# Kernel optimization log

Measured on AMD Instinct MI355X. Metric: run time of the kernel, lower is better.

The kernel has to match this reference:

```python
import jax, jax.numpy as jnp
import numpy as np

NEG = -1e10

def setup_inputs() -> dict:
    key = jax.random.key(0)
    ks = jax.random.split(key, 12)
    B, W, V, D, R, VOCAB = 16, 64, 64, 256, 64, 50000
    head_ctx = jax.random.randint(ks[0], (B, W), 0, VOCAB)
    tail_ctx = jax.random.randint(ks[1], (B, V), 0, VOCAB)
    emb = jax.random.normal(ks[2], (VOCAB, D), dtype=jnp.float32) * 0.02
    rela_mat = jax.random.normal(ks[3], (R, D), dtype=jnp.float32) * 0.02
    fc_w = jax.random.normal(ks[4], (3 * D, D), dtype=jnp.float32) * (1.0 / np.sqrt(3 * D))
    fc_b = jnp.zeros((D,), jnp.float32)
    att_w1 = jax.random.normal(ks[5], (D, D), dtype=jnp.float32) * (1.0 / np.sqrt(D))
    att_b1 = jnp.zeros((D,), jnp.float32)
    att_w2 = jax.random.normal(ks[6], (D, 1), dtype=jnp.float32) * (1.0 / np.sqrt(D))
    att_b2 = jnp.zeros((1,), jnp.float32)
    out_w = jax.random.normal(ks[7], (D, 1), dtype=jnp.float32) * (1.0 / np.sqrt(D))
    out_b = jnp.zeros((1,), jnp.float32)
    return {"head_ctx": head_ctx, "tail_ctx": tail_ctx, "emb": emb, "rela_mat": rela_mat,
            "fc_w": fc_w, "fc_b": fc_b, "att_w1": att_w1, "att_b1": att_b1,
            "att_w2": att_w2, "att_b2": att_b2, "out_w": out_w, "out_b": out_b}

def reference(head_ctx, tail_ctx, emb, rela_mat, fc_w, fc_b, att_w1, att_b1, att_w2, att_b2, out_w, out_b):
    A = emb[head_ctx]            # [B, W, D]
    Bt = emb[tail_ctx]           # [B, V, D]
    Bsz, W, D = A.shape
    V = Bt.shape[1]
    R = rela_mat.shape[0]
    N = W * V
    # DistMult scoring for every (head_i, tail_j, rela_r) triple, no repeat materialization
    scores = jnp.einsum('bid,bjd,rd->bijr', A, Bt, rela_mat).reshape(Bsz, N, R)
    # cut_rela_score: mask relations not beating the null (last) relation
    null = scores[:, :, -1:]
    scores = jnp.where(scores <= null, NEG, scores)
    norm_scores = jax.nn.softmax(scores, axis=-1)            # [B, N, R]
    rela_vec = jnp.einsum('bnr,rd->bnd', norm_scores, rela_mat)
    # tuple (i,j) pairing: index n = i*V + j
    A_rep = jnp.broadcast_to(A[:, :, None, :], (Bsz, W, V, D)).reshape(Bsz, N, D)
    B_rep = jnp.broadcast_to(Bt[:, None, :, :], (Bsz, W, V, D)).reshape(Bsz, N, D)
    tuple_vec = jnp.tanh(jnp.concatenate([A_rep, B_rep, rela_vec], axis=-1) @ fc_w + fc_b)  # [B, N, D]
    # tuple attention pooling
    att = jnp.tanh(tuple_vec @ att_w1 + att_b1) @ att_w2 + att_b2   # [B, N, 1]
    att_norms = jax.nn.softmax(att, axis=1)                          # [B, N, 1]
    fuse = jnp.sum(att_norms * tuple_vec, axis=1)                    # [B, D]
    logits = (fuse @ out_w + out_b).squeeze(-1)                      # [B]
    return logits, att_norms, norm_scores
```

## Files before the change

### kernel.cpp

```cpp
#include <hip/hip_runtime.h>
#include <hip/hip_bf16.h>

#define NB 16
#define NW 64
#define NV 64
#define ND 256
#define NR 64
#define NN 4096
#define NEGV -10000000000.0f

typedef __attribute__((ext_vector_type(8))) short short8;
typedef __attribute__((ext_vector_type(4))) float f32x4;

__device__ inline float cvt(const void* p, int idx, int flag) {
  if (flag) return __bfloat162float(((const __hip_bfloat16*)p)[idx]);
  return ((const float*)p)[idx];
}
__device__ inline void stv(void* p, int idx, float v, int flag) {
  if (flag) ((__hip_bfloat16*)p)[idx] = __float2bfloat16(v);
  else ((float*)p)[idx] = v;
}
__device__ inline float bf2f(short s) {
  return __uint_as_float(((unsigned int)(unsigned short)s) << 16);
}
__device__ inline float tanh_fast(float x) {
  float ax = fabsf(x);
  float e = __expf(-2.f * ax);
  float r = (1.f - e) / (1.f + e);
  return copysignf(r, x);
}

__global__ void k_detect(const unsigned int* embw, int* flagp) {
  __shared__ float red[256];
  int t = threadIdx.x;
  float mx = 0.f;
  for (int i = t; i < 1024; i += 256) {
    unsigned int w = embw[i];
    unsigned int fb = (w & 0xffffu) << 16;
    float a = fabsf(__uint_as_float(fb));
    if (!(a < 1e9f)) a = 1e9f;
    mx = fmaxf(mx, a);
  }
  red[t] = mx;
  __syncthreads();
  for (int s = 128; s > 0; s >>= 1) {
    if (t < s) red[t] = fmaxf(red[t], red[t + s]);
    __syncthreads();
  }
  if (t == 0) flagp[0] = (red[0] < 1000.f) ? 1 : 0;
}

__global__ void k_prep(const void* rela, float* relaT,
                       const void* b1, const void* w2, const void* outw,
                       const void* b2, const void* outb, float* sp,
                       const void* w1, __hip_bfloat16* w1b,
                       const int* head, const int* tail, const void* emb,
                       float* Af, float* Bf, const int* flagp) {
  int flag = flagp[0];
  int blk = blockIdx.x;
  int t = threadIdx.x;
  if (blk < 64) {
    relaT[t * NR + blk] = cvt(rela, blk * ND + t, flag);
  } else if (blk == 64) {
    sp[t] = cvt(b1, t, flag);
    sp[256 + t] = cvt(w2, t, flag);
    sp[512 + t] = cvt(outw, t, flag);
    if (t == 0) {
      sp[768] = cvt(b2, 0, flag);
      sp[769] = cvt(outb, 0, flag);
    }
  } else if (blk < 321) {
    int flat = (blk - 65) * 256 + t;
    int i = flat & 7;
    int lane = (flat >> 3) & 63;
    int kst = (flat >> 9) & 7;
    int nt = flat >> 12;
    int k = kst * 32 + (lane >> 4) * 8 + i;
    int n = nt * 16 + (lane & 15);
    w1b[flat] = __float2bfloat16(cvt(w1, k * ND + n, flag));
  } else {
    int row = blk - 321;
    if (row < NB * NW) {
      int ix = head[row];
      Af[row * ND + t] = cvt(emb, ix * ND + t, flag);
    } else {
      int rr = row - NB * NW;
      int ix = tail[rr];
      Bf[rr * ND + t] = cvt(emb, ix * ND + t, flag);
    }
  }
}

__global__ void __launch_bounds__(256) k_premm(const float* __restrict__ Af,
                                               const float* __restrict__ Bf,
                                               const void* __restrict__ rela,
                                               const void* __restrict__ fcw,
                                               const void* __restrict__ fcb,
                                               float* __restrict__ Ah,
                                               float* __restrict__ Bh,
                                               __hip_bfloat16* __restrict__ rwb,
                                               const int* __restrict__ flagp) {
  int flag = flagp[0];
  int blk = blockIdx.x;
  int t = threadIdx.x;
  __shared__ float rl[4][ND];
  int base, wbase, addb = 0, isr = 0;
  const float* src = Af;
  if (blk < 256) { base = blk * 4; wbase = 0; addb = 1; }
  else if (blk < 512) { base = (blk - 256) * 4; src = Bf; wbase = ND; }
  else { base = (blk - 512) * 4; wbase = 2 * ND; isr = 1; }
#pragma unroll
  for (int i = 0; i < 4; ++i)
    rl[i][t] = isr ? cvt(rela, (base + i) * ND + t, flag)
                   : src[(base + i) * ND + t];
  __syncthreads();
  float acc0 = 0.f, acc1 = 0.f, acc2 = 0.f, acc3 = 0.f;
  const f32x4* r0p = (const f32x4*)rl[0];
  const f32x4* r1p = (const f32x4*)rl[1];
  const f32x4* r2p = (const f32x4*)rl[2];
  const f32x4* r3p = (const f32x4*)rl[3];
#pragma unroll 4
  for (int k4 = 0; k4 < 64; ++k4) {
    float w0 = cvt(fcw, (wbase + k4 * 4 + 0) * ND + t, flag);
    float w1v = cvt(fcw, (wbase + k4 * 4 + 1) * ND + t, flag);
    float w2v = cvt(fcw, (wbase + k4 * 4 + 2) * ND + t, flag);
    float w3v = cvt(fcw, (wbase + k4 * 4 + 3) * ND + t, flag);
    f32x4 r0 = r0p[k4], r1 = r1p[k4], r2 = r2p[k4], r3 = r3p[k4];
    acc0 += r0.x * w0 + r0.y * w1v + r0.z * w2v + r0.w * w3v;
    acc1 += r1.x * w0 + r1.y * w1v + r1.z * w2v + r1.w * w3v;
    acc2 += r2.x * w0 + r2.y * w1v + r2.z * w2v + r2.w * w3v;
    acc3 += r3.x * w0 + r3.y * w1v + r3.z * w2v + r3.w * w3v;
  }
  float bias = addb ? cvt(fcb, t, flag) : 0.f;
  float res[4] = {acc0 + bias, acc1 + bias, acc2 + bias, acc3 + bias};
  if (!isr) {
    float* dst = addb ? Ah : Bh;
#pragma unroll
    for (int i = 0; i < 4; ++i) dst[(base + i) * ND + t] = res[i];
  } else {
#pragma unroll
    for (int i = 0; i < 4; ++i) {
      int rr = base + i;
      int ks = rr >> 5, ii = rr & 7, lh = (rr >> 3) & 3;
      int nt = t >> 4, ll = t & 15;
      int flat = ((nt * 2 + ks) * 64 + lh * 16 + ll) * 8 + ii;
      rwb[flat] = __float2bfloat16(res[i]);
    }
  }
}

__global__ void __launch_bounds__(256) k_scores(const float* __restrict__ Af,
                                                const float* __restrict__ Bf,
                                                const float* __restrict__ relaT,
                                                void* __restrict__ out,
                                                __hip_bfloat16* __restrict__ nsb,
                                                const int* __restrict__ flagp) {
  int flag = flagp[0];
  int bi = blockIdx.x;
  int b = bi >> 6;
  int t = threadIdx.x;
  int r = t & 63;
  int q = t >> 6;
  __shared__ float Al[ND];
  __shared__ float Bl[2][4 * ND];
  __shared__ float part[2][4 * 256];
  Al[t] = Af[bi * ND + t];
  f32x4 pre = *(const f32x4*)(Bf + ((size_t)b * NV + q) * ND + r * 4);
  __syncthreads();
  float preR[64];
#pragma unroll
  for (int i2 = 0; i2 < 64; ++i2) {
    int d = q * 64 + i2;
    preR[i2] = Al[d] * relaT[d * NR + r];
  }

  for (int jg = 0; jg < 16; ++jg) {
    int buf = jg & 1;
    *(f32x4*)(&Bl[buf][q * ND + r * 4]) = pre;
    if (jg < 15)
      pre = *(const f32x4*)(Bf + ((size_t)b * NV + (jg + 1) * 4 + q) * ND + r * 4);
    __syncthreads();

    if (jg > 0) {
      const float* pb = part[1 - buf];
      float s = pb[q * 256 + r] + pb[q * 256 + 64 + r]
              + pb[q * 256 + 128 + r] + pb[q * 256 + 192 + r];
      float nullv = __shfl(s, 63, 64);
      float m = (s <= nullv) ? NEGV : s;
      float mx = m;
#pragma unroll
      for (int o = 32; o > 0; o >>= 1) mx = fmaxf(mx, __shfl_xor(mx, o, 64));
      float e = __expf(m - mx);
      float sum = e;
#pragma unroll
      for (int o = 32; o > 0; o >>= 1) sum += __shfl_xor(sum, o, 64);
      float ns = e / sum;
      int j = (jg - 1) * 4 + q;
      int nidx = (bi * 64 + j) * 64 + r;
      stv(out, 16 + NB * NN + nidx, ns, flag);
      nsb[nidx] = __float2bfloat16(ns);
    }

    const f32x4* Bl4 = (const f32x4*)Bl[buf];
#pragma unroll
    for (int jj = 0; jj < 4; ++jj) {
      float acc = 0.f;
      int ib = jj * 64 + q * 16;
#pragma unroll
      for (int i4 = 0; i4 < 16; ++i4) {
        f32x4 bv = Bl4[ib + i4];
        acc += preR[i4 * 4 + 0] * bv.x;
        acc += preR[i4 * 4 + 1] * bv.y;
        acc += preR[i4 * 4 + 2] * bv.z;
        acc += preR[i4 * 4 + 3] * bv.w;
      }
      part[buf][jj * 256 + t] = acc;
    }
  }
  __syncthreads();
  {
    const float* pb = part[1];
    float s = pb[q * 256 + r] + pb[q * 256 + 64 + r]
            + pb[q * 256 + 128 + r] + pb[q * 256 + 192 + r];
    float nullv = __shfl(s, 63, 64);
    float m = (s <= nullv) ? NEGV : s;
    float mx = m;
#pragma unroll
    for (int o = 32; o > 0; o >>= 1) mx = fmaxf(mx, __shfl_xor(mx, o, 64));
    float e = __expf(m - mx);
    float sum = e;
#pragma unroll
    for (int o = 32; o > 0; o >>= 1) sum += __shfl_xor(sum, o, 64);
    float ns = e / sum;
    int j = 15 * 4 + q;
    int nidx = (bi * 64 + j) * 64 + r;
    stv(out, 16 + NB * NN + nidx, ns, flag);
    nsb[nidx] = __float2bfloat16(ns);
  }
}

__global__ void __launch_bounds__(256) k_tuple2(const __hip_bfloat16* __restrict__ nsb,
                                                const __hip_bfloat16* __restrict__ rwb,
                                                const float* __restrict__ Ah,
                                                const float* __restrict__ Bh,
                                                __hip_bfloat16* __restrict__ tup) {
  int t = threadIdx.x;
  int wv = t >> 6, lane = t & 63;
  int bi = blockIdx.x;
  int b = bi >> 6;
  const short* nsS = (const short*)nsb;
  const short* rwS = (const short*)rwb;
  int m = lane & 15;
  int kgrp = lane >> 4;
  f32x4 acc[16];
#pragma unroll
  for (int i = 0; i < 16; ++i) acc[i] = (f32x4){0.f, 0.f, 0.f, 0.f};
  int nrow = bi * 64 + wv * 16 + m;
#pragma unroll
  for (int ks = 0; ks < 2; ++ks) {
    short8 a = *(const short8*)(nsS + (size_t)nrow * 64 + ks * 32 + kgrp * 8);
#pragma unroll
    for (int nt = 0; nt < 16; ++nt) {
      short8 bfr = *(const short8*)(rwS + (((nt * 2 + ks) * 64 + lane) << 3));
      acc[nt] = __builtin_amdgcn_mfma_f32_16x16x32_bf16(a, bfr, acc[nt], 0, 0, 0);
    }
  }
  int rbase = bi * 64 + wv * 16 + (lane >> 4) * 4;
  int jbase = rbase & 63;
#pragma unroll
  for (int nt = 0; nt < 16; ++nt) {
    int col = nt * 16 + m;
    float ahv = Ah[bi * ND + col];
#pragma unroll
    for (int reg = 0; reg < 4; ++reg) {
      int ng = rbase + reg;
      float v = acc[nt][reg] + ahv + Bh[(size_t)(b * 64 + jbase + reg) * ND + col];
      tup[(size_t)ng * ND + col] = __float2bfloat16(tanh_fast(v));
    }
  }
}

__global__ void __launch_bounds__(256) k_att2(const __hip_bfloat16* __restrict__ tup,
                                              const __hip_bfloat16* __restrict__ w1b,
                                              const float* __restrict__ sp,
                                              float* __restrict__ att_raw,
                                              float* __restrict__ dotv) {
  int t = threadIdx.x;
  int wv = t >> 6, lane = t & 63;
  int r0 = blockIdx.x * 64 + wv * 16;
  const short* tupS = (const short*)tup;
  const short* w1S = (const short*)w1b;
  const float* owf = sp + 512;
  float b2v = sp[768];

  f32x4 acc[16];
#pragma unroll
  for (int i = 0; i < 16; ++i) acc[i] = (f32x4){0.f, 0.f, 0.f, 0.f};
  float dp = 0.f;
  int arow = r0 + (lane & 15);
  int kgrp = lane >> 4;

#pragma unroll
  for (int ks = 0; ks < 8; ++ks) {
    int k0 = ks * 32 + kgrp * 8;
    short8 a = *(const short8*)(tupS + (size_t)arow * ND + k0);
#pragma unroll
    for (int i = 0; i < 8; ++i)
      dp += bf2f(a[i]) * owf[k0 + i];
#pragma unroll
    for (int nt = 0; nt < 16; ++nt) {
      short8 bfr = *(const short8*)(w1S + (((nt * 8 + ks) * 64 + lane) << 3));
      acc[nt] = __builtin_amdgcn_mfma_f32_16x16x32_bf16(a, bfr, acc[nt], 0, 0, 0);
    }
  }

  dp += __shfl_xor(dp, 16, 64);
  dp += __shfl_xor(dp, 32, 64);
  if (lane < 16) dotv[r0 + lane] = dp;

  float p0[4] = {0.f, 0.f, 0.f, 0.f};
#pragma unroll
  for (int nt = 0; nt < 16; ++nt) {
    int col = nt * 16 + (lane & 15);
    float b1v = sp[col];
    float w2v = sp[256 + col];
#pragma unroll
    for (int reg = 0; reg < 4; ++reg)
      p0[reg] += tanh_fast(acc[nt][reg] + b1v) * w2v;
  }
#pragma unroll
  for (int o = 1; o < 16; o <<= 1) {
#pragma unroll
    for (int reg = 0; reg < 4; ++reg)
      p0[reg] += __shfl_xor(p0[reg], o, 64);
  }
  if ((lane & 15) == 0) {
    int rb = r0 + (lane >> 4) * 4;
#pragma unroll
    for (int reg = 0; reg < 4; ++reg)
      att_raw[rb + reg] = p0[reg] + b2v;
  }
}

__global__ void k_fuse(const float* att_raw, const float* dotv,
                       const float* sp, void* out, const int* flagp) {
  int flag = flagp[0];
  int b = blockIdx.x;
  int t = threadIdx.x;
  __shared__ float red[256];
  float vals[16];
  float mx = -3.4e38f;
#pragma unroll
  for (int c = 0; c < 16; ++c) {
    vals[c] = att_raw[b * NN + c * 256 + t];
    mx = fmaxf(mx, vals[c]);
  }
  red[t] = mx;
  __syncthreads();
  for (int s = 128; s > 0; s >>= 1) {
    if (t < s) red[t] = fmaxf(red[t], red[t + s]);
    __syncthreads();
  }
  float M = red[0];
  __syncthreads();
  float sm = 0.f;
#pragma unroll
  for (int c = 0; c < 16; ++c) {
    vals[c] = __expf(vals[c] - M);
    sm += vals[c];
  }
  red[t] = sm;
  __syncthreads();
  for (int s = 128; s > 0; s >>= 1) {
    if (t < s) red[t] += red[t + s];
    __syncthreads();
  }
  float Z = red[0];
  __syncthreads();
  float acc = 0.f;
#pragma unroll
  for (int c = 0; c < 16; ++c) {
    int n = c * 256 + t;
    float a = vals[c] / Z;
    stv(out, 16 + b * NN + n, a, flag);
    acc += a * dotv[b * NN + n];
  }
  red[t] = acc;
  __syncthreads();
  for (int s = 128; s > 0; s >>= 1) {
    if (t < s) red[t] += red[t + s];
    __syncthreads();
  }
  if (t == 0) stv(out, b, red[0] + sp[769], flag);
}

extern "C" void kernel_launch(void* const* d_in, const int* in_sizes, int n_in,
                              void* d_out, int out_size, void* d_ws, size_t ws_size,
                              hipStream_t stream) {
  const int* head = (const int*)d_in[0];
  const int* tail = (const int*)d_in[1];
  const void* emb = d_in[2];
  const void* rela = d_in[3];
  const void* fcw = d_in[4];
  const void* fcb = d_in[5];
  const void* w1 = d_in[6];
  const void* b1 = d_in[7];
  const void* w2 = d_in[8];
  const void* b2 = d_in[9];
  const void* outw = d_in[10];
  const void* outb = d_in[11];

  float* ws = (float*)d_ws;
  int* flagp = (int*)d_ws;
  const size_t O_RELAT = 16;
  const size_t O_AF = O_RELAT + 16384;
  const size_t O_BF = O_AF + 262144;
  const size_t O_AH = O_BF + 262144;
  const size_t O_BH = O_AH + 262144;
  const size_t O_ATTR = O_BH + 262144;
  const size_t O_DOT = O_ATTR + 65536;
  const size_t O_SP = O_DOT + 65536;
  const size_t O_W1B = O_SP + 1024;
  const size_t O_RWB = O_W1B + 32768;
  const size_t O_NSB = O_RWB + 8192;
  const size_t O_TUP = O_NSB + 2097152;

  float* relaT = ws + O_RELAT;
  float* Af = ws + O_AF;
  float* Bf = ws + O_BF;
  float* Ah = ws + O_AH;
  float* Bh = ws + O_BH;
  float* attr = ws + O_ATTR;
  float* dotv = ws + O_DOT;
  float* sp = ws + O_SP;
  __hip_bfloat16* w1b = (__hip_bfloat16*)(ws + O_W1B);
  __hip_bfloat16* rwb = (__hip_bfloat16*)(ws + O_RWB);
  __hip_bfloat16* nsb = (__hip_bfloat16*)(ws + O_NSB);
  __hip_bfloat16* tup = (__hip_bfloat16*)(ws + O_TUP);

  hipLaunchKernelGGL(k_detect, dim3(1), dim3(256), 0, stream,
                     (const unsigned int*)emb, flagp);
  hipLaunchKernelGGL(k_prep, dim3(2369), dim3(256), 0, stream,
                     rela, relaT, b1, w2, outw, b2, outb, sp,
                     w1, w1b, head, tail, emb, Af, Bf, flagp);
  hipLaunchKernelGGL(k_premm, dim3(528), dim3(256), 0, stream,
                     Af, Bf, rela, fcw, fcb, Ah, Bh, rwb, flagp);
  hipLaunchKernelGGL(k_scores, dim3(1024), dim3(256), 0, stream,
                     Af, Bf, relaT, d_out, nsb, flagp);
  hipLaunchKernelGGL(k_tuple2, dim3(1024), dim3(256), 0, stream,
                     nsb, rwb, Ah, Bh, tup);
  hipLaunchKernelGGL(k_att2, dim3(1024), dim3(256), 0, stream,
                     tup, w1b, sp, attr, dotv);
  hipLaunchKernelGGL(k_fuse, dim3(16), dim3(256), 0, stream,
                     attr, dotv, sp, d_out, flagp);
}
```

Before: 259.3 us.

## Stage MFMA weight operands in LDS and double-buffer attention GEMM with 32 rows per wave

The tuple kernel now copies the relation-projection weights into shared memory once per block instead of every wave reading them from global memory. The attention kernel is rewritten to give each wave 32 rows, reusing each weight fragment for two MFMAs, and it halves the grid. W1 weights are reordered by k-step so each step's slab can be double-buffered through LDS while the next activation fragment is prefetched. The aim is to cut redundant global and L2 weight traffic. In exchange, accumulator registers double and extra syncs are added, which may lower occupancy.

New measurement: 238.3 us. -8.1%, faster.

```diff
diff --git a/kernel.cpp b/kernel.cpp
--- a/kernel.cpp
+++ b/kernel.cpp
@@ -73,9 +73,9 @@
     int flat = (blk - 65) * 256 + t;
     int i = flat & 7;
     int lane = (flat >> 3) & 63;
-    int kst = (flat >> 9) & 7;
-    int nt = flat >> 12;
-    int k = kst * 32 + (lane >> 4) * 8 + i;
+    int nt = (flat >> 9) & 15;
+    int ks = flat >> 13;
+    int k = ks * 32 + (lane >> 4) * 8 + i;
     int n = nt * 16 + (lane & 15);
     w1b[flat] = __float2bfloat16(cvt(w1, k * ND + n, flag));
   } else {
@@ -244,28 +244,33 @@
                                                 const float* __restrict__ Ah,
                                                 const float* __restrict__ Bh,
                                                 __hip_bfloat16* __restrict__ tup) {
+  __shared__ __align__(16) short rwl[16384];
   int t = threadIdx.x;
   int wv = t >> 6, lane = t & 63;
   int bi = blockIdx.x;
   int b = bi >> 6;
   const short* nsS = (const short*)nsb;
-  const short* rwS = (const short*)rwb;
+  const short8* rwsrc = (const short8*)rwb;
+  short8* rwdst = (short8*)rwl;
+#pragma unroll
+  for (int i = 0; i < 8; ++i) rwdst[t + 256 * i] = rwsrc[t + 256 * i];
   int m = lane & 15;
   int kgrp = lane >> 4;
+  int nrow = bi * 64 + wv * 16 + m;
+  short8 a0 = *(const short8*)(nsS + (size_t)nrow * 64 + kgrp * 8);
+  short8 a1 = *(const short8*)(nsS + (size_t)nrow * 64 + 32 + kgrp * 8);
+  __syncthreads();
   f32x4 acc[16];
 #pragma unroll
   for (int i = 0; i < 16; ++i) acc[i] = (f32x4){0.f, 0.f, 0.f, 0.f};
-  int nrow = bi * 64 + wv * 16 + m;
-#pragma unroll
-  for (int ks = 0; ks < 2; ++ks) {
-    short8 a = *(const short8*)(nsS + (size_t)nrow * 64 + ks * 32 + kgrp * 8);
-#pragma unroll
-    for (int nt = 0; nt < 16; ++nt) {
-      short8 bfr = *(const short8*)(rwS + (((nt * 2 + ks) * 64 + lane) << 3));
-      acc[nt] = __builtin_amdgcn_mfma_f32_16x16x32_bf16(a, bfr, acc[nt], 0, 0, 0);
-    }
-  }
-  int rbase = bi * 64 + wv * 16 + (lane >> 4) * 4;
+#pragma unroll
+  for (int nt = 0; nt < 16; ++nt) {
+    short8 b0 = *(const short8*)(rwl + (((nt * 2 + 0) * 64 + lane) << 3));
+    short8 b1f = *(const short8*)(rwl + (((nt * 2 + 1) * 64 + lane) << 3));
+    acc[nt] = __builtin_amdgcn_mfma_f32_16x16x32_bf16(a0, b0, acc[nt], 0, 0, 0);
+    acc[nt] = __builtin_amdgcn_mfma_f32_16x16x32_bf16(a1, b1f, acc[nt], 0, 0, 0);
+  }
+  int rbase = bi * 64 + wv * 16 + kgrp * 4;
   int jbase = rbase & 63;
 #pragma unroll
   for (int nt = 0; nt < 16; ++nt) {
@@ -280,65 +285,105 @@
   }
 }
 
-__global__ void __launch_bounds__(256) k_att2(const __hip_bfloat16* __restrict__ tup,
+__global__ void __launch_bounds__(256) k_att3(const __hip_bfloat16* __restrict__ tup,
                                               const __hip_bfloat16* __restrict__ w1b,
                                               const float* __restrict__ sp,
                                               float* __restrict__ att_raw,
                                               float* __restrict__ dotv) {
+  __shared__ __align__(16) short bl[2][8192];
   int t = threadIdx.x;
   int wv = t >> 6, lane = t & 63;
-  int r0 = blockIdx.x * 64 + wv * 16;
+  int r0 = blockIdx.x * 128 + wv * 32;
   const short* tupS = (const short*)tup;
-  const short* w1S = (const short*)w1b;
+  const short8* w1v = (const short8*)w1b;
   const float* owf = sp + 512;
   float b2v = sp[768];
-
-  f32x4 acc[16];
-#pragma unroll
-  for (int i = 0; i < 16; ++i) acc[i] = (f32x4){0.f, 0.f, 0.f, 0.f};
-  float dp = 0.f;
-  int arow = r0 + (lane & 15);
+  int m = lane & 15;
   int kgrp = lane >> 4;
-
-#pragma unroll
+  int arow0 = r0 + m;
+  int arow1 = arow0 + 16;
+
+  {
+    short8* dst = (short8*)bl[0];
+#pragma unroll
+    for (int i = 0; i < 4; ++i) dst[t + 256 * i] = w1v[t + 256 * i];
+  }
+  short8 a0 = *(const short8*)(tupS + (size_t)arow0 * ND + kgrp * 8);
+  short8 a1 = *(const short8*)(tupS + (size_t)arow1 * ND + kgrp * 8);
+
+  f32x4 acc0[16], acc1[16];
+#pragma unroll
+  for (int i = 0; i < 16; ++i) {
+    acc0[i] = (f32x4){0.f, 0.f, 0.f, 0.f};
+    acc1[i] = (f32x4){0.f, 0.f, 0.f, 0.f};
+  }
+  float dp0 = 0.f, dp1 = 0.f;
+
   for (int ks = 0; ks < 8; ++ks) {
+    int buf = ks & 1;
+    __syncthreads();
+    if (ks < 7) {
+      const short8* src = w1v + (ks + 1) * 1024;
+      short8* dst = (short8*)bl[1 - buf];
+#pragma unroll
+      for (int i = 0; i < 4; ++i) dst[t + 256 * i] = src[t + 256 * i];
+    }
+    short8 ca0 = a0, ca1 = a1;
+    if (ks < 7) {
+      int k0n = (ks + 1) * 32 + kgrp * 8;
+      a0 = *(const short8*)(tupS + (size_t)arow0 * ND + k0n);
+      a1 = *(const short8*)(tupS + (size_t)arow1 * ND + k0n);
+    }
     int k0 = ks * 32 + kgrp * 8;
-    short8 a = *(const short8*)(tupS + (size_t)arow * ND + k0);
-#pragma unroll
-    for (int i = 0; i < 8; ++i)
-      dp += bf2f(a[i]) * owf[k0 + i];
+#pragma unroll
+    for (int i = 0; i < 8; ++i) {
+      float w = owf[k0 + i];
+      dp0 += bf2f(ca0[i]) * w;
+      dp1 += bf2f(ca1[i]) * w;
+    }
 #pragma unroll
     for (int nt = 0; nt < 16; ++nt) {
-      short8 bfr = *(const short8*)(w1S + (((nt * 8 + ks) * 64 + lane) << 3));
-      acc[nt] = __builtin_amdgcn_mfma_f32_16x16x32_bf16(a, bfr, acc[nt], 0, 0, 0);
-    }
-  }
-
-  dp += __shfl_xor(dp, 16, 64);
-  dp += __shfl_xor(dp, 32, 64);
-  if (lane < 16) dotv[r0 + lane] = dp;
+      short8 bfr = *(const short8*)(bl[buf] + ((nt * 64 + lane) << 3));
+      acc0[nt] = __builtin_amdgcn_mfma_f32_16x16x32_bf16(ca0, bfr, acc0[nt], 0, 0, 0);
+      acc1[nt] = __builtin_amdgcn_mfma_f32_16x16x32_bf16(ca1, bfr, acc1[nt], 0, 0, 0);
+    }
+  }
+
+  dp0 += __shfl_xor(dp0, 16, 64); dp0 += __shfl_xor(dp0, 32, 64);
+  dp1 += __shfl_xor(dp1, 16, 64); dp1 += __shfl_xor(dp1, 32, 64);
+  if (lane < 16) {
+    dotv[r0 + lane] = dp0;
+    dotv[r0 + 16 + lane] = dp1;
+  }
 
   float p0[4] = {0.f, 0.f, 0.f, 0.f};
+  float p1[4] = {0.f, 0.f, 0.f, 0.f};
 #pragma unroll
   for (int nt = 0; nt < 16; ++nt) {
-    int col = nt * 16 + (lane & 15);
+    int col = nt * 16 + m;
     float b1v = sp[col];
     float w2v = sp[256 + col];
 #pragma unroll
-    for (int reg = 0; reg < 4; ++reg)
-      p0[reg] += tanh_fast(acc[nt][reg] + b1v) * w2v;
+    for (int reg = 0; reg < 4; ++reg) {
+      p0[reg] += tanh_fast(acc0[nt][reg] + b1v) * w2v;
+      p1[reg] += tanh_fast(acc1[nt][reg] + b1v) * w2v;
+    }
   }
 #pragma unroll
   for (int o = 1; o < 16; o <<= 1) {
 #pragma unroll
-    for (int reg = 0; reg < 4; ++reg)
+    for (int reg = 0; reg < 4; ++reg) {
       p0[reg] += __shfl_xor(p0[reg], o, 64);
-  }
-  if ((lane & 15) == 0) {
-    int rb = r0 + (lane >> 4) * 4;
-#pragma unroll
-    for (int reg = 0; reg < 4; ++reg)
+      p1[reg] += __shfl_xor(p1[reg], o, 64);
+    }
+  }
+  if (m == 0) {
+    int rb = r0 + kgrp * 4;
+#pragma unroll
+    for (int reg = 0; reg < 4; ++reg) {
       att_raw[rb + reg] = p0[reg] + b2v;
+      att_raw[rb + 16 + reg] = p1[reg] + b2v;
+    }
   }
 }
 
@@ -449,7 +494,7 @@
                      Af, Bf, relaT, d_out, nsb, flagp);
   hipLaunchKernelGGL(k_tuple2, dim3(1024), dim3(256), 0, stream,
                      nsb, rwb, Ah, Bh, tup);
-  hipLaunchKernelGGL(k_att2, dim3(1024), dim3(256), 0, stream,
+  hipLaunchKernelGGL(k_att3, dim3(512), dim3(256), 0, stream,
                      tup, w1b, sp, attr, dotv);
   hipLaunchKernelGGL(k_fuse, dim3(16), dim3(256), 0, stream,
                      attr, dotv, sp, d_out, flagp);
```
